# Kernel tuning notes

Measured on AMD Instinct MI355X. Metric: run time of the kernel, lower is better.

Reference implementation:

```python
import jax, jax.numpy as jnp
import numpy as np

D = 64        # state dim (num_output)
H = 256       # MLP hidden width
B = 4096      # batch
NUM_STEPS = 16  # fixed-step Dormand-Prince steps over t in [0,1] per bijector


def _mlp(t, y, W1, b1, W2, b2, W3, b3):
    # time-conditioned MLP: concat scalar t to state, two tanh layers, linear out
    tcol = jnp.full((y.shape[0], 1), t, dtype=y.dtype)
    h = jnp.tanh(jnp.concatenate([y, tcol], axis=1) @ W1 + b1)
    h = jnp.tanh(h @ W2 + b2)
    return h @ W3 + b3


def _dopri5_fixed(f, y0):
    # classic Dormand-Prince (RK45) Butcher tableau, 5th-order solution,
    # fixed step h = 1/NUM_STEPS from t=0 to t=1
    h = jnp.asarray(1.0 / NUM_STEPS, dtype=y0.dtype)

    def step(y, i):
        t = i.astype(y0.dtype) * h
        k1 = f(t, y)
        k2 = f(t + h * (1/5),  y + h * ((1/5) * k1))
        k3 = f(t + h * (3/10), y + h * ((3/40) * k1 + (9/40) * k2))
        k4 = f(t + h * (4/5),  y + h * ((44/45) * k1 - (56/15) * k2 + (32/9) * k3))
        k5 = f(t + h * (8/9),  y + h * ((19372/6561) * k1 - (25360/2187) * k2
                                        + (64448/6561) * k3 - (212/729) * k4))
        k6 = f(t + h,          y + h * ((9017/3168) * k1 - (355/33) * k2
                                        + (46732/5247) * k3 + (49/176) * k4
                                        - (5103/18656) * k5))
        y_next = y + h * ((35/384) * k1 + (500/1113) * k3 + (125/192) * k4
                          - (2187/6784) * k5 + (11/84) * k6)
        return y_next, None

    y_final, _ = jax.lax.scan(step, y0, jnp.arange(NUM_STEPS))
    return y_final


def setup_inputs() -> dict:
    key = jax.random.key(0)
    ks = jax.random.split(key, 7)
    s_in = 1.0 / np.sqrt(D + 1)
    s_h = 1.0 / np.sqrt(H)
    inp = {"x": jax.random.normal(ks[0], (B, D), dtype=jnp.float32)}
    for i, base in enumerate([1, 4]):
        inp[f"p{i}_W1"] = jax.random.normal(ks[base], (D + 1, H), dtype=jnp.float32) * s_in
        inp[f"p{i}_b1"] = jnp.zeros((H,), dtype=jnp.float32)
        inp[f"p{i}_W2"] = jax.random.normal(ks[base + 1], (H, H), dtype=jnp.float32) * s_h
        inp[f"p{i}_b2"] = jnp.zeros((H,), dtype=jnp.float32)
        inp[f"p{i}_W3"] = jax.random.normal(ks[base + 2], (H, D), dtype=jnp.float32) * s_h
        inp[f"p{i}_b3"] = jnp.zeros((D,), dtype=jnp.float32)
    return inp


def reference(x, p0_W1, p0_b1, p0_W2, p0_b2, p0_W3, p0_b3,
              p1_W1, p1_b1, p1_W2, p1_b2, p1_W3, p1_b3):
    # Chain(list(reversed(bijectors))).forward applies bijector 0 first, then 1.
    # FFJORD bijector forward = integrate dz/dt = mlp(t, z) from t=0 to t=1.
    y = x
    params = [(p0_W1, p0_b1, p0_W2, p0_b2, p0_W3, p0_b3),
              (p1_W1, p1_b1, p1_W2, p1_b2, p1_W3, p1_b3)]
    for (W1, b1, W2, b2, W3, b3) in params:
        f = lambda t, z: _mlp(t, z, W1, b1, W2, b2, W3, b3)
        y = _dopri5_fixed(f, y)
    return y
```

## Files before the change

kernel.cpp:

```cpp
#include <hip/hip_runtime.h>

typedef __attribute__((ext_vector_type(8))) short short8;
typedef __attribute__((ext_vector_type(4))) float f32x4;

#define NSTEPS 16

__device__ __forceinline__ unsigned short bf16rne(float f) {
  unsigned int u = __float_as_uint(f);
  u += 0x7FFFu + ((u >> 16) & 1u);
  return (unsigned short)(u >> 16);
}

#if __has_builtin(__builtin_amdgcn_cvt_pk_bf16_f32)
typedef __attribute__((ext_vector_type(2))) __bf16 v2bf16;
__device__ __forceinline__ unsigned int pk2(float a, float b) {
  v2bf16 t = __builtin_amdgcn_cvt_pk_bf16_f32(a, b);
  unsigned int r;
  __builtin_memcpy(&r, &t, 4);
  return r;
}
#else
__device__ __forceinline__ unsigned int pk2(float a, float b) {
  unsigned int ua = __float_as_uint(a), ub = __float_as_uint(b);
  ua += 0x7FFFu + ((ua >> 16) & 1u);
  ub += 0x7FFFu + ((ub >> 16) & 1u);
  return (ua >> 16) | (ub & 0xFFFF0000u);
}
#endif

__device__ __forceinline__ float tanh_fast(float x) {
  float e = __builtin_amdgcn_exp2f(x * 2.8853900817779268f);
  return __builtin_fmaf(-2.0f, __builtin_amdgcn_rcpf(e + 1.0f), 1.0f);
}

__global__ void ffjord_setup(const float* __restrict__ W1a, const float* __restrict__ W2a,
                             const float* __restrict__ W3a, const float* __restrict__ W1b,
                             const float* __restrict__ W2b, const float* __restrict__ W3b,
                             unsigned short* __restrict__ ws) {
  int gid = blockIdx.x * blockDim.x + threadIdx.x;
  int bij = gid / 12288;
  int r = gid - bij * 12288;
  const float* W1 = bij ? W1b : W1a;
  const float* W2 = bij ? W2b : W2a;
  const float* W3 = bij ? W3b : W3a;
  unsigned short* o = ws + bij * 98304;
  const float* src;
  int kstride;
  if (r < 2048) {
    int lane = r & 63, nt = (r >> 6) & 15, ks = r >> 10;
    int k0 = ks * 32 + (lane >> 4) * 8, n = nt * 16 + (lane & 15);
    src = W1 + k0 * 256 + n; kstride = 256; o += r * 8;
  } else if (r < 10240) {
    int rr = r - 2048;
    int lane = rr & 63, nt = (rr >> 6) & 15, ks = rr >> 10;
    int k0 = ks * 32 + (lane >> 4) * 8, n = nt * 16 + (lane & 15);
    src = W2 + k0 * 256 + n; kstride = 256; o += 16384 + rr * 8;
  } else {
    int rr = r - 10240;
    int lane = rr & 63, nt = (rr >> 6) & 3, ks = rr >> 8;
    int k0 = ks * 32 + (lane >> 4) * 8, n = nt * 16 + (lane & 15);
    src = W3 + k0 * 64 + n; kstride = 64; o += 81920 + rr * 8;
  }
  #pragma unroll
  for (int j = 0; j < 8; j++) o[j] = bf16rne(src[j * kstride]);
}

__global__ __launch_bounds__(1024, 4) void ffjord_main(
    const float* __restrict__ x, float* __restrict__ out,
    const unsigned short* __restrict__ ws,
    const float* __restrict__ W1a, const float* __restrict__ b1a,
    const float* __restrict__ b2a, const float* __restrict__ b3a,
    const float* __restrict__ W1b, const float* __restrict__ b1b,
    const float* __restrict__ b2b, const float* __restrict__ b3b) {
  __shared__ __align__(16) unsigned short zA[1088];
  __shared__ __align__(16) unsigned short h1A[4096];
  __shared__ __align__(16) unsigned short h2A[4096];
  __shared__ __align__(16) float fbuf[4][16 * 68];

  const int tid = threadIdx.x;
  const int wave = tid >> 6;
  const int lane = tid & 63;
  const int cl = lane & 15;
  const int qd = lane >> 4;
  const int mt3 = wave & 3;
  const int kq = wave >> 2;
  const int c3 = mt3 * 16 + qd * 4;
  const int row0 = blockIdx.x * 16;
  const int row = wave;
  const int d0 = lane;

  const int zoff = ((d0 >> 5) * 4 + ((d0 >> 3) & 3)) * 136 + row * 8 + (d0 & 7);
  const int zrb = qd * 136 + cl * 8;
  const int c0 = wave * 16 + qd * 4;
  const int hoff = (c0 >> 5) * 512 + ((c0 & 31) >> 3) * 128 + cl * 8 + (c0 & 7);

  const float hstep = 1.0f / 16.0f;

  float y = x[(row0 + row) * 64 + d0];
  float k[6];

  const float ACO[6][5] = {
      {0.f, 0.f, 0.f, 0.f, 0.f},
      {1.f / 5.f, 0.f, 0.f, 0.f, 0.f},
      {3.f / 40.f, 9.f / 40.f, 0.f, 0.f, 0.f},
      {44.f / 45.f, -56.f / 15.f, 32.f / 9.f, 0.f, 0.f},
      {19372.f / 6561.f, -25360.f / 2187.f, 64448.f / 6561.f, -212.f / 729.f, 0.f},
      {9017.f / 3168.f, -355.f / 33.f, 46732.f / 5247.f, 49.f / 176.f, -5103.f / 18656.f}};
  const float CT[6] = {0.0f, 0.2f, 0.3f, 0.8f, 8.0f / 9.0f, 1.0f};
  const float BW0 = 35.f / 384.f, BW2 = 500.f / 1113.f, BW3 = 125.f / 192.f,
              BW4 = -2187.f / 6784.f, BW5 = 11.f / 84.f;

  for (int bij = 0; bij < 2; bij++) {
    const unsigned short* wsb = ws + bij * 98304;
    const float* W1 = bij ? W1b : W1a;
    const float* b1 = bij ? b1b : b1a;
    const float* b2 = bij ? b2b : b2a;
    const float* b3 = bij ? b3b : b3a;

    f32x4 b1c = *(const f32x4*)(b1 + c0);
    f32x4 w1t4 = *(const f32x4*)(W1 + 64 * 256 + c0);
    f32x4 b2c = *(const f32x4*)(b2 + c0);
    f32x4 b3c;
    if (kq == 0) b3c = *(const f32x4*)(b3 + c3);
    else { b3c[0] = 0.f; b3c[1] = 0.f; b3c[2] = 0.f; b3c[3] = 0.f; }

    const short8* w1p = (const short8*)wsb;
    const short8* w2p = (const short8*)(wsb + 16384);
    const short8* w3p = (const short8*)(wsb + 81920);
    short8 w1f[2];
    #pragma unroll
    for (int ks = 0; ks < 2; ks++)
      w1f[ks] = w1p[(ks * 16 + wave) * 64 + lane];
    short8 w2f[8];
    #pragma unroll
    for (int ks = 0; ks < 8; ks++)
      w2f[ks] = w2p[(ks * 16 + wave) * 64 + lane];
    short8 w3f[2];
    #pragma unroll
    for (int kk = 0; kk < 2; kk++)
      w3f[kk] = w3p[((kq * 2 + kk) * 4 + mt3) * 64 + lane];

    for (int step = 0; step < NSTEPS; step++) {
      float stepf = (float)step;
      #pragma unroll
      for (int s = 0; s < 6; s++) {
        float ts = (stepf + CT[s]) * hstep;

        {
          float z = y;
          #pragma unroll
          for (int j = 0; j < 5; j++)
            if (j < s) z += (hstep * ACO[s][j]) * k[j];
          zA[zoff] = bf16rne(z);
        }
        __syncthreads();

        {
          short8 a0 = *(const short8*)(zA + zrb);
          short8 a1 = *(const short8*)(zA + zrb + 544);
          f32x4 acc;
          #pragma unroll
          for (int r = 0; r < 4; r++)
            acc[r] = __builtin_fmaf(ts, w1t4[r], b1c[r]);
          acc = __builtin_amdgcn_mfma_f32_16x16x32_bf16(w1f[0], a0, acc, 0, 0, 0);
          acc = __builtin_amdgcn_mfma_f32_16x16x32_bf16(w1f[1], a1, acc, 0, 0, 0);
          uint2 pv;
          pv.x = pk2(tanh_fast(acc[0]), tanh_fast(acc[1]));
          pv.y = pk2(tanh_fast(acc[2]), tanh_fast(acc[3]));
          *(uint2*)(h1A + hoff) = pv;
        }
        __syncthreads();

        {
          f32x4 accA = b2c;
          f32x4 accB; accB[0] = 0.f; accB[1] = 0.f; accB[2] = 0.f; accB[3] = 0.f;
          #pragma unroll
          for (int ks = 0; ks < 4; ks++) {
            short8 hb = ((const short8*)h1A)[ks * 64 + lane];
            accA = __builtin_amdgcn_mfma_f32_16x16x32_bf16(w2f[ks], hb, accA, 0, 0, 0);
          }
          #pragma unroll
          for (int ks = 4; ks < 8; ks++) {
            short8 hb = ((const short8*)h1A)[ks * 64 + lane];
            accB = __builtin_amdgcn_mfma_f32_16x16x32_bf16(w2f[ks], hb, accB, 0, 0, 0);
          }
          uint2 pv;
          pv.x = pk2(tanh_fast(accA[0] + accB[0]), tanh_fast(accA[1] + accB[1]));
          pv.y = pk2(tanh_fast(accA[2] + accB[2]), tanh_fast(accA[3] + accB[3]));
          *(uint2*)(h2A + hoff) = pv;
        }
        __syncthreads();

        {
          short8 hb0 = ((const short8*)h2A)[(kq * 2 + 0) * 64 + lane];
          short8 hb1 = ((const short8*)h2A)[(kq * 2 + 1) * 64 + lane];
          f32x4 accP = b3c;
          accP = __builtin_amdgcn_mfma_f32_16x16x32_bf16(w3f[0], hb0, accP, 0, 0, 0);
          accP = __builtin_amdgcn_mfma_f32_16x16x32_bf16(w3f[1], hb1, accP, 0, 0, 0);
          *(f32x4*)(&fbuf[kq][cl * 68 + c3]) = accP;
        }
        __syncthreads();

        {
          int fo = row * 68 + d0;
          k[s] = (fbuf[0][fo] + fbuf[1][fo]) + (fbuf[2][fo] + fbuf[3][fo]);
        }
      }

      y += hstep * (BW0 * k[0] + BW2 * k[2] + BW3 * k[3] + BW4 * k[4] + BW5 * k[5]);
    }
  }

  out[(row0 + row) * 64 + d0] = y;
}

extern "C" void kernel_launch(void* const* d_in, const int* in_sizes, int n_in,
                              void* d_out, int out_size, void* d_ws, size_t ws_size,
                              hipStream_t stream) {
  (void)in_sizes; (void)n_in; (void)out_size; (void)ws_size;
  const float* x   = (const float*)d_in[0];
  const float* W1a = (const float*)d_in[1];
  const float* b1a = (const float*)d_in[2];
  const float* W2a = (const float*)d_in[3];
  const float* b2a = (const float*)d_in[4];
  const float* W3a = (const float*)d_in[5];
  const float* b3a = (const float*)d_in[6];
  const float* W1b = (const float*)d_in[7];
  const float* b1b = (const float*)d_in[8];
  const float* W2b = (const float*)d_in[9];
  const float* b2b = (const float*)d_in[10];
  const float* W3b = (const float*)d_in[11];
  const float* b3b = (const float*)d_in[12];
  unsigned short* ws = (unsigned short*)d_ws;
  float* out = (float*)d_out;

  hipLaunchKernelGGL(ffjord_setup, dim3(96), dim3(256), 0, stream,
                     W1a, W2a, W3a, W1b, W2b, W3b, ws);
  hipLaunchKernelGGL(ffjord_main, dim3(256), dim3(1024), 0, stream,
                     x, out, ws, W1a, b1a, b2a, b3a, W1b, b1b, b2b, b3b);
}
```

Measured before the change: 327.1 us.

## Fuse layer-3 reduction and RK stage update into four waves, dropping a barrier

The layer-3 matmul is restructured so four waves each compute the full K=256 reduction for 16 output columns, with W3 staged in shared memory. This removes the cross-wave fbuf reduction and one __syncthreads per stage. Those waves also keep the ODE state and k-values in their MFMA accumulator layout and write the next stage's bf16 input directly. The other 12 waves sit idle during layer 3, and the extra 32KB of LDS for W3 may reduce occupancy.

```diff
diff --git a/kernel.cpp b/kernel.cpp
--- a/kernel.cpp
+++ b/kernel.cpp
@@ -75,32 +75,28 @@
   __shared__ __align__(16) unsigned short zA[1088];
   __shared__ __align__(16) unsigned short h1A[4096];
   __shared__ __align__(16) unsigned short h2A[4096];
-  __shared__ __align__(16) float fbuf[4][16 * 68];
+  __shared__ __align__(16) unsigned short w3s[16384];
 
   const int tid = threadIdx.x;
   const int wave = tid >> 6;
   const int lane = tid & 63;
   const int cl = lane & 15;
   const int qd = lane >> 4;
-  const int mt3 = wave & 3;
-  const int kq = wave >> 2;
-  const int c3 = mt3 * 16 + qd * 4;
   const int row0 = blockIdx.x * 16;
-  const int row = wave;
-  const int d0 = lane;
-
-  const int zoff = ((d0 >> 5) * 4 + ((d0 >> 3) & 3)) * 136 + row * 8 + (d0 & 7);
-  const int zrb = qd * 136 + cl * 8;
+
   const int c0 = wave * 16 + qd * 4;
   const int hoff = (c0 >> 5) * 512 + ((c0 & 31) >> 3) * 128 + cl * 8 + (c0 & 7);
+  const int zrb = qd * 136 + cl * 8;
+  const int w3i = wave & 3;
+  const int dl3 = w3i * 16 + qd * 4;
+  const int zw = (2 * w3i + (qd >> 1)) * 136 + cl * 8 + 4 * (qd & 1);
 
   const float hstep = 1.0f / 16.0f;
 
-  float y = x[(row0 + row) * 64 + d0];
-  float k[6];
-
-  const float ACO[6][5] = {
-      {0.f, 0.f, 0.f, 0.f, 0.f},
+  float kreg[6][4];
+  f32x4 yc;
+
+  const float A2[5][5] = {
       {1.f / 5.f, 0.f, 0.f, 0.f, 0.f},
       {3.f / 40.f, 9.f / 40.f, 0.f, 0.f, 0.f},
       {44.f / 45.f, -56.f / 15.f, 32.f / 9.f, 0.f, 0.f},
@@ -120,13 +116,10 @@
     f32x4 b1c = *(const f32x4*)(b1 + c0);
     f32x4 w1t4 = *(const f32x4*)(W1 + 64 * 256 + c0);
     f32x4 b2c = *(const f32x4*)(b2 + c0);
-    f32x4 b3c;
-    if (kq == 0) b3c = *(const f32x4*)(b3 + c3);
-    else { b3c[0] = 0.f; b3c[1] = 0.f; b3c[2] = 0.f; b3c[3] = 0.f; }
+    f32x4 b3c = *(const f32x4*)(b3 + dl3);
 
     const short8* w1p = (const short8*)wsb;
     const short8* w2p = (const short8*)(wsb + 16384);
-    const short8* w3p = (const short8*)(wsb + 81920);
     short8 w1f[2];
     #pragma unroll
     for (int ks = 0; ks < 2; ks++)
@@ -135,25 +128,28 @@
     #pragma unroll
     for (int ks = 0; ks < 8; ks++)
       w2f[ks] = w2p[(ks * 16 + wave) * 64 + lane];
-    short8 w3f[2];
-    #pragma unroll
-    for (int kk = 0; kk < 2; kk++)
-      w3f[kk] = w3p[((kq * 2 + kk) * 4 + mt3) * 64 + lane];
+
+    {
+      const uint4* s4 = (const uint4*)(wsb + 81920);
+      uint4* d4 = (uint4*)w3s;
+      d4[tid] = s4[tid];
+      d4[tid + 1024] = s4[tid + 1024];
+    }
+
+    if (bij == 0 && wave < 4) {
+      yc = *(const f32x4*)(x + (row0 + cl) * 64 + dl3);
+      uint2 pv;
+      pv.x = pk2(yc[0], yc[1]);
+      pv.y = pk2(yc[2], yc[3]);
+      *(uint2*)(zA + zw) = pv;
+    }
+    __syncthreads();
 
     for (int step = 0; step < NSTEPS; step++) {
       float stepf = (float)step;
       #pragma unroll
       for (int s = 0; s < 6; s++) {
         float ts = (stepf + CT[s]) * hstep;
-
-        {
-          float z = y;
-          #pragma unroll
-          for (int j = 0; j < 5; j++)
-            if (j < s) z += (hstep * ACO[s][j]) * k[j];
-          zA[zoff] = bf16rne(z);
-        }
-        __syncthreads();
 
         {
           short8 a0 = *(const short8*)(zA + zrb);
@@ -191,27 +187,51 @@
         }
         __syncthreads();
 
-        {
-          short8 hb0 = ((const short8*)h2A)[(kq * 2 + 0) * 64 + lane];
-          short8 hb1 = ((const short8*)h2A)[(kq * 2 + 1) * 64 + lane];
+        if (wave < 4) {
           f32x4 accP = b3c;
-          accP = __builtin_amdgcn_mfma_f32_16x16x32_bf16(w3f[0], hb0, accP, 0, 0, 0);
-          accP = __builtin_amdgcn_mfma_f32_16x16x32_bf16(w3f[1], hb1, accP, 0, 0, 0);
-          *(f32x4*)(&fbuf[kq][cl * 68 + c3]) = accP;
+          f32x4 accQ; accQ[0] = 0.f; accQ[1] = 0.f; accQ[2] = 0.f; accQ[3] = 0.f;
+          #pragma unroll
+          for (int ks = 0; ks < 8; ks += 2) {
+            short8 hb0 = ((const short8*)h2A)[ks * 64 + lane];
+            short8 wf0 = ((const short8*)w3s)[(ks * 4 + w3i) * 64 + lane];
+            short8 hb1 = ((const short8*)h2A)[(ks + 1) * 64 + lane];
+            short8 wf1 = ((const short8*)w3s)[((ks + 1) * 4 + w3i) * 64 + lane];
+            accP = __builtin_amdgcn_mfma_f32_16x16x32_bf16(wf0, hb0, accP, 0, 0, 0);
+            accQ = __builtin_amdgcn_mfma_f32_16x16x32_bf16(wf1, hb1, accQ, 0, 0, 0);
+          }
+          #pragma unroll
+          for (int r = 0; r < 4; r++) kreg[s][r] = accP[r] + accQ[r];
+
+          f32x4 z;
+          if (s < 5) {
+            #pragma unroll
+            for (int r = 0; r < 4; r++) {
+              float v = yc[r];
+              #pragma unroll
+              for (int j = 0; j < 5; j++)
+                if (j <= s) v += (hstep * A2[s][j]) * kreg[j][r];
+              z[r] = v;
+            }
+          } else {
+            #pragma unroll
+            for (int r = 0; r < 4; r++) {
+              yc[r] += hstep * (BW0 * kreg[0][r] + BW2 * kreg[2][r] + BW3 * kreg[3][r] +
+                                BW4 * kreg[4][r] + BW5 * kreg[5][r]);
+              z[r] = yc[r];
+            }
+          }
+          uint2 pv;
+          pv.x = pk2(z[0], z[1]);
+          pv.y = pk2(z[2], z[3]);
+          *(uint2*)(zA + zw) = pv;
         }
         __syncthreads();
-
-        {
-          int fo = row * 68 + d0;
-          k[s] = (fbuf[0][fo] + fbuf[1][fo]) + (fbuf[2][fo] + fbuf[3][fo]);
-        }
       }
-
-      y += hstep * (BW0 * k[0] + BW2 * k[2] + BW3 * k[3] + BW4 * k[4] + BW5 * k[5]);
     }
   }
 
-  out[(row0 + row) * 64 + d0] = y;
+  if (wave < 4)
+    *(f32x4*)(out + (row0 + cl) * 64 + dl3) = yc;
 }
 
 extern "C" void kernel_launch(void* const* d_in, const int* in_sizes, int n_in,
```

Measured after the change: 329.7 us. No clear change (+0.8%).
